# Optimization experiments

Measured on AMD Instinct MI355X. Metric: run time of the kernel, lower is better.

## Reference

```python
import jax, jax.numpy as jnp
import numpy as np
from jax import lax

B, T, N, FI, FO, K = 32, 128, 200, 32, 64, 3
STRIDE, PAD, DIL = 1, 1, 1


def setup_inputs() -> dict:
    key = jax.random.key(0)
    k1, k2, k3 = jax.random.split(key, 3)
    bound = 1.0 / np.sqrt(FI * K)
    x = jax.random.normal(k1, (B, T, N, FI), dtype=jnp.float32)
    weight = jax.random.uniform(k2, (N * FO, FI, K), dtype=jnp.float32,
                                minval=-bound, maxval=bound)
    bias = jax.random.uniform(k3, (N, FO), dtype=jnp.float32,
                              minval=-bound, maxval=bound)
    return {"x": x, "weight": weight, "bias": bias}


def reference(x, weight, bias):
    # x: [B, T, N, FI] -> [B, N*FI, T]   (rearrange '... t n f -> ... (n f) t')
    b, t, n, fi = x.shape
    fo = bias.shape[1]
    xc = jnp.transpose(x, (0, 2, 3, 1)).reshape(b, n * fi, t)
    # Grouped conv1d: one group per instance (n groups), weight [N*FO, FI, K]
    out = lax.conv_general_dilated(
        xc, weight,
        window_strides=(STRIDE,),
        padding=[(PAD, PAD)],
        rhs_dilation=(DIL,),
        feature_group_count=n,
        dimension_numbers=("NCH", "OIH", "NCH"),
    )  # [B, N*FO, T_out]
    t_out = out.shape[-1]
    # rearrange '... (n f) t -> ... t n f'
    out = jnp.transpose(out.reshape(b, n, fo, t_out), (0, 3, 1, 2))
    return out + bias  # bias broadcasts over [B, T_out, N, FO]
```

## Files before the change

### kernel.cpp

```cpp
#include <hip/hip_runtime.h>
#include <hip/hip_bf16.h>
#include <cstddef>

#define B_ 32
#define T_ 128
#define N_ 200
#define FI_ 32
#define FO_ 64
#define K_ 3

typedef __attribute__((ext_vector_type(8))) short short8;
typedef __attribute__((ext_vector_type(8))) unsigned short ushort8;
typedef __attribute__((ext_vector_type(4))) float f32x4;

#define AROW_ 40
#define A_ROWS_ (T_ + 2)
#define B_OFF_ (A_ROWS_ * AROW_)
#define BROW_ 40
#define BK_SZ_ (FO_ * BROW_)

__device__ __forceinline__ unsigned short f2bf(float f) {
    union { __hip_bfloat16 h; unsigned short u; } cv;
    cv.h = __float2bfloat16(f);
    return cv.u;
}

__global__ __launch_bounds__(256, 4) void multiconv_mfma(
    const float* __restrict__ x, const float* __restrict__ w,
    const float* __restrict__ bias, float* __restrict__ out)
{
    __shared__ __align__(16) unsigned short lds[B_OFF_ + K_ * BK_SZ_];

    const int bid = blockIdx.x;
    const int b = bid & 31;
    const int n = bid >> 5;
    const int tid = threadIdx.x;
    const int lane = tid & 63;
    const int wv = tid >> 6;

    const float* xb = x + ((size_t)b * T_ * N_ + n) * FI_;
    for (int s = tid; s < A_ROWS_ * 4; s += 256) {
        const int rr = s >> 2, q = s & 3;
        const int t = rr - 1;
        ushort8 u = (ushort8)0;
        if (t >= 0 && t < T_) {
            const float4 v0 = *reinterpret_cast<const float4*>(
                &xb[(size_t)t * N_ * FI_ + q * 8]);
            const float4 v1 = *reinterpret_cast<const float4*>(
                &xb[(size_t)t * N_ * FI_ + q * 8 + 4]);
            u[0] = f2bf(v0.x); u[1] = f2bf(v0.y); u[2] = f2bf(v0.z); u[3] = f2bf(v0.w);
            u[4] = f2bf(v1.x); u[5] = f2bf(v1.y); u[6] = f2bf(v1.z); u[7] = f2bf(v1.w);
        }
        *reinterpret_cast<ushort8*>(&lds[rr * AROW_ + q * 8]) = u;
    }

    {
        const int f = tid >> 2;
        const int i0 = (tid & 3) * 8;
        const float* wp = w + ((size_t)n * FO_ + f) * (FI_ * K_) + (size_t)i0 * K_;
        float v[24];
        #pragma unroll
        for (int j = 0; j < 6; ++j) {
            const float4 t4 = *reinterpret_cast<const float4*>(&wp[j * 4]);
            v[j*4+0] = t4.x; v[j*4+1] = t4.y; v[j*4+2] = t4.z; v[j*4+3] = t4.w;
        }
        #pragma unroll
        for (int k = 0; k < K_; ++k) {
            ushort8 u;
            #pragma unroll
            for (int j = 0; j < 8; ++j) u[j] = f2bf(v[j * K_ + k]);
            *reinterpret_cast<ushort8*>(&lds[B_OFF_ + k * BK_SZ_ + f * BROW_ + i0]) = u;
        }
    }

    __syncthreads();

    f32x4 acc[2][4];
    #pragma unroll
    for (int m = 0; m < 2; ++m)
        #pragma unroll
        for (int j = 0; j < 4; ++j)
            acc[m][j] = (f32x4){0.f, 0.f, 0.f, 0.f};

    const int row16 = lane & 15;
    const int grp = lane >> 4;

    #pragma unroll
    for (int k = 0; k < K_; ++k) {
        const short8 a0 = *reinterpret_cast<const short8*>(
            &lds[(wv * 32 + 0  + row16 + k) * AROW_ + grp * 8]);
        const short8 a1 = *reinterpret_cast<const short8*>(
            &lds[(wv * 32 + 16 + row16 + k) * AROW_ + grp * 8]);
        #pragma unroll
        for (int j = 0; j < 4; ++j) {
            const short8 bf = *reinterpret_cast<const short8*>(
                &lds[B_OFF_ + k * BK_SZ_ + (j * 16 + row16) * BROW_ + grp * 8]);
            acc[0][j] = __builtin_amdgcn_mfma_f32_16x16x32_bf16(a0, bf, acc[0][j], 0, 0, 0);
            acc[1][j] = __builtin_amdgcn_mfma_f32_16x16x32_bf16(a1, bf, acc[1][j], 0, 0, 0);
        }
    }

    #pragma unroll
    for (int j = 0; j < 4; ++j) {
        const float bv = bias[n * FO_ + j * 16 + row16];
        #pragma unroll
        for (int m = 0; m < 2; ++m) {
            #pragma unroll
            for (int r = 0; r < 4; ++r) {
                const int t = wv * 32 + m * 16 + grp * 4 + r;
                out[(((size_t)b * T_ + t) * N_ + n) * FO_ + j * 16 + row16] =
                    acc[m][j][r] + bv;
            }
        }
    }
}

extern "C" void kernel_launch(void* const* d_in, const int* in_sizes, int n_in,
                              void* d_out, int out_size, void* d_ws, size_t ws_size,
                              hipStream_t stream) {
    const float* x    = (const float*)d_in[0];
    const float* w    = (const float*)d_in[1];
    const float* bias = (const float*)d_in[2];
    float* out = (float*)d_out;

    const int grid = B_ * N_;
    multiconv_mfma<<<grid, 256, 0, stream>>>(x, w, bias, out);
}
```

Baseline: 78.59 us.

## Process two batches per block with double-buffered input prefetch

Each block now handles two batch elements for one instance. The weight tile is converted to bf16 once and reused for both, halving weight loading and conversion. The second batch's input is loaded into registers while the first tile is computed, then written to a second LDS buffer. This halves the grid size and raises LDS use and register pressure (six float4 prefetch registers), which may reduce occupancy.

```diff
diff --git a/kernel.cpp b/kernel.cpp
--- a/kernel.cpp
+++ b/kernel.cpp
@@ -8,6 +8,7 @@
 #define FI_ 32
 #define FO_ 64
 #define K_ 3
+#define NB_ 2
 
 typedef __attribute__((ext_vector_type(8))) short short8;
 typedef __attribute__((ext_vector_type(8))) unsigned short ushort8;
@@ -15,14 +16,62 @@
 
 #define AROW_ 40
 #define A_ROWS_ (T_ + 2)
-#define B_OFF_ (A_ROWS_ * AROW_)
+#define ABUF_ (A_ROWS_ * AROW_)
+#define B_OFF_ (2 * ABUF_)
 #define BROW_ 40
 #define BK_SZ_ (FO_ * BROW_)
+#define NSLOT_ (A_ROWS_ * 4)
 
 __device__ __forceinline__ unsigned short f2bf(float f) {
     union { __hip_bfloat16 h; unsigned short u; } cv;
     cv.h = __float2bfloat16(f);
     return cv.u;
+}
+
+__device__ __forceinline__ f32x4 mfma16(short8 a, short8 b, f32x4 c) {
+    return __builtin_amdgcn_mfma_f32_16x16x32_bf16(a, b, c, 0, 0, 0);
+}
+
+__device__ __forceinline__ void compute_tile(
+    const unsigned short* __restrict__ lds, int abase,
+    int wv, int lane, f32x4 acc[2][4])
+{
+    const int row16 = lane & 15;
+    const int grp = lane >> 4;
+    #pragma unroll
+    for (int k = 0; k < K_; ++k) {
+        const short8 a0 = *reinterpret_cast<const short8*>(
+            &lds[abase + (wv * 32 + 0  + row16 + k) * AROW_ + grp * 8]);
+        const short8 a1 = *reinterpret_cast<const short8*>(
+            &lds[abase + (wv * 32 + 16 + row16 + k) * AROW_ + grp * 8]);
+        #pragma unroll
+        for (int j = 0; j < 4; ++j) {
+            const short8 bf = *reinterpret_cast<const short8*>(
+                &lds[B_OFF_ + k * BK_SZ_ + (j * 16 + row16) * BROW_ + grp * 8]);
+            acc[0][j] = mfma16(a0, bf, acc[0][j]);
+            acc[1][j] = mfma16(a1, bf, acc[1][j]);
+        }
+    }
+}
+
+__device__ __forceinline__ void store_tile(
+    float* __restrict__ out, int b, int n, int wv, int lane,
+    const float bvj[4], f32x4 acc[2][4])
+{
+    const int row16 = lane & 15;
+    const int grp = lane >> 4;
+    #pragma unroll
+    for (int j = 0; j < 4; ++j) {
+        #pragma unroll
+        for (int m = 0; m < 2; ++m) {
+            #pragma unroll
+            for (int r = 0; r < 4; ++r) {
+                const int t = wv * 32 + m * 16 + grp * 4 + r;
+                out[(((size_t)b * T_ + t) * N_ + n) * FO_ + j * 16 + row16] =
+                    acc[m][j][r] + bvj[j];
+            }
+        }
+    }
 }
 
 __global__ __launch_bounds__(256, 4) void multiconv_mfma(
@@ -32,27 +81,13 @@
     __shared__ __align__(16) unsigned short lds[B_OFF_ + K_ * BK_SZ_];
 
     const int bid = blockIdx.x;
-    const int b = bid & 31;
-    const int n = bid >> 5;
+    const int n = bid % N_;
+    const int bp = bid / N_;
+    const int b0 = bp * NB_;
+    const int b1 = b0 + 1;
     const int tid = threadIdx.x;
     const int lane = tid & 63;
     const int wv = tid >> 6;
-
-    const float* xb = x + ((size_t)b * T_ * N_ + n) * FI_;
-    for (int s = tid; s < A_ROWS_ * 4; s += 256) {
-        const int rr = s >> 2, q = s & 3;
-        const int t = rr - 1;
-        ushort8 u = (ushort8)0;
-        if (t >= 0 && t < T_) {
-            const float4 v0 = *reinterpret_cast<const float4*>(
-                &xb[(size_t)t * N_ * FI_ + q * 8]);
-            const float4 v1 = *reinterpret_cast<const float4*>(
-                &xb[(size_t)t * N_ * FI_ + q * 8 + 4]);
-            u[0] = f2bf(v0.x); u[1] = f2bf(v0.y); u[2] = f2bf(v0.z); u[3] = f2bf(v0.w);
-            u[4] = f2bf(v1.x); u[5] = f2bf(v1.y); u[6] = f2bf(v1.z); u[7] = f2bf(v1.w);
-        }
-        *reinterpret_cast<ushort8*>(&lds[rr * AROW_ + q * 8]) = u;
-    }
 
     {
         const int f = tid >> 2;
@@ -73,46 +108,83 @@
         }
     }
 
+    const float* xb0 = x + ((size_t)b0 * T_ * N_ + n) * FI_;
+    const float* xb1 = x + ((size_t)b1 * T_ * N_ + n) * FI_;
+    #pragma unroll
+    for (int ss = 0; ss < 3; ++ss) {
+        const int s = tid + ss * 256;
+        if (ss < 2 || tid < NSLOT_ - 512) {
+            const int rr = s >> 2, q = s & 3;
+            const int t = rr - 1;
+            ushort8 u = (ushort8)0;
+            if (t >= 0 && t < T_) {
+                const float4 v0 = *reinterpret_cast<const float4*>(
+                    &xb0[(size_t)t * N_ * FI_ + q * 8]);
+                const float4 v1 = *reinterpret_cast<const float4*>(
+                    &xb0[(size_t)t * N_ * FI_ + q * 8 + 4]);
+                u[0] = f2bf(v0.x); u[1] = f2bf(v0.y); u[2] = f2bf(v0.z); u[3] = f2bf(v0.w);
+                u[4] = f2bf(v1.x); u[5] = f2bf(v1.y); u[6] = f2bf(v1.z); u[7] = f2bf(v1.w);
+            }
+            *reinterpret_cast<ushort8*>(&lds[rr * AROW_ + q * 8]) = u;
+        }
+    }
+
     __syncthreads();
 
+    float4 nv[6];
+    #pragma unroll
+    for (int ss = 0; ss < 3; ++ss) {
+        const int s = tid + ss * 256;
+        if (ss < 2 || tid < NSLOT_ - 512) {
+            const int rr = s >> 2, q = s & 3;
+            const int t = rr - 1;
+            if (t >= 0 && t < T_) {
+                nv[ss*2]   = *reinterpret_cast<const float4*>(
+                    &xb1[(size_t)t * N_ * FI_ + q * 8]);
+                nv[ss*2+1] = *reinterpret_cast<const float4*>(
+                    &xb1[(size_t)t * N_ * FI_ + q * 8 + 4]);
+            }
+        }
+    }
+
+    const int row16 = lane & 15;
+    float bvj[4];
+    #pragma unroll
+    for (int j = 0; j < 4; ++j) bvj[j] = bias[n * FO_ + j * 16 + row16];
+
     f32x4 acc[2][4];
     #pragma unroll
     for (int m = 0; m < 2; ++m)
         #pragma unroll
-        for (int j = 0; j < 4; ++j)
-            acc[m][j] = (f32x4){0.f, 0.f, 0.f, 0.f};
-
-    const int row16 = lane & 15;
-    const int grp = lane >> 4;
-
-    #pragma unroll
-    for (int k = 0; k < K_; ++k) {
-        const short8 a0 = *reinterpret_cast<const short8*>(
-            &lds[(wv * 32 + 0  + row16 + k) * AROW_ + grp * 8]);
-        const short8 a1 = *reinterpret_cast<const short8*>(
-            &lds[(wv * 32 + 16 + row16 + k) * AROW_ + grp * 8]);
-        #pragma unroll
-        for (int j = 0; j < 4; ++j) {
-            const short8 bf = *reinterpret_cast<const short8*>(
-                &lds[B_OFF_ + k * BK_SZ_ + (j * 16 + row16) * BROW_ + grp * 8]);
-            acc[0][j] = __builtin_amdgcn_mfma_f32_16x16x32_bf16(a0, bf, acc[0][j], 0, 0, 0);
-            acc[1][j] = __builtin_amdgcn_mfma_f32_16x16x32_bf16(a1, bf, acc[1][j], 0, 0, 0);
-        }
-    }
-
-    #pragma unroll
-    for (int j = 0; j < 4; ++j) {
-        const float bv = bias[n * FO_ + j * 16 + row16];
-        #pragma unroll
-        for (int m = 0; m < 2; ++m) {
-            #pragma unroll
-            for (int r = 0; r < 4; ++r) {
-                const int t = wv * 32 + m * 16 + grp * 4 + r;
-                out[(((size_t)b * T_ + t) * N_ + n) * FO_ + j * 16 + row16] =
-                    acc[m][j][r] + bv;
-            }
-        }
-    }
+        for (int j = 0; j < 4; ++j) acc[m][j] = (f32x4){0.f, 0.f, 0.f, 0.f};
+    compute_tile(lds, 0, wv, lane, acc);
+
+    #pragma unroll
+    for (int ss = 0; ss < 3; ++ss) {
+        const int s = tid + ss * 256;
+        if (ss < 2 || tid < NSLOT_ - 512) {
+            const int rr = s >> 2, q = s & 3;
+            const int t = rr - 1;
+            ushort8 u = (ushort8)0;
+            if (t >= 0 && t < T_) {
+                const float4 v0 = nv[ss*2], v1 = nv[ss*2+1];
+                u[0] = f2bf(v0.x); u[1] = f2bf(v0.y); u[2] = f2bf(v0.z); u[3] = f2bf(v0.w);
+                u[4] = f2bf(v1.x); u[5] = f2bf(v1.y); u[6] = f2bf(v1.z); u[7] = f2bf(v1.w);
+            }
+            *reinterpret_cast<ushort8*>(&lds[ABUF_ + rr * AROW_ + q * 8]) = u;
+        }
+    }
+
+    store_tile(out, b0, n, wv, lane, bvj, acc);
+
+    __syncthreads();
+
+    #pragma unroll
+    for (int m = 0; m < 2; ++m)
+        #pragma unroll
+        for (int j = 0; j < 4; ++j) acc[m][j] = (f32x4){0.f, 0.f, 0.f, 0.f};
+    compute_tile(lds, ABUF_, wv, lane, acc);
+    store_tile(out, b1, n, wv, lane, bvj, acc);
 }
 
 extern "C" void kernel_launch(void* const* d_in, const int* in_sizes, int n_in,
@@ -123,6 +195,6 @@
     const float* bias = (const float*)d_in[2];
     float* out = (float*)d_out;
 
-    const int grid = B_ * N_;
+    const int grid = (B_ / NB_) * N_;
     multiconv_mfma<<<grid, 256, 0, stream>>>(x, w, bias, out);
 }
```

New measurement: 89.48 us. 13.8% more time.

## Pre-convert weights to bf16 and tile conv by time chunks without LDS

Applied to the files above, without the earlier changes.

Adds a prep kernel that converts the weights once per call into a bf16 layout in the workspace, arranged per tap. The main kernel is retiled so each block covers a 16-step time chunk for 25 instances, with each wave looping over instances. Each wave loads its A and B fragments straight from global memory into registers, dropping LDS and __syncthreads. The aim is better output-write locality and no per-block weight conversion, at the cost of an extra launch, re-reading x for each tap, and possible wave imbalance (25 instances over 4 waves).

```diff
diff --git a/kernel.cpp b/kernel.cpp
--- a/kernel.cpp
+++ b/kernel.cpp
@@ -8,16 +8,12 @@
 #define FI_ 32
 #define FO_ 64
 #define K_ 3
+#define TT_ 16
+#define NPB_ 25
 
 typedef __attribute__((ext_vector_type(8))) short short8;
 typedef __attribute__((ext_vector_type(8))) unsigned short ushort8;
 typedef __attribute__((ext_vector_type(4))) float f32x4;
-
-#define AROW_ 40
-#define A_ROWS_ (T_ + 2)
-#define B_OFF_ (A_ROWS_ * AROW_)
-#define BROW_ 40
-#define BK_SZ_ (FO_ * BROW_)
 
 __device__ __forceinline__ unsigned short f2bf(float f) {
     union { __hip_bfloat16 h; unsigned short u; } cv;
@@ -25,91 +21,109 @@
     return cv.u;
 }
 
-__global__ __launch_bounds__(256, 4) void multiconv_mfma(
+__global__ void conv_prep(const float* __restrict__ w,
+                          unsigned short* __restrict__ wbf) {
+    const int idx = blockIdx.x * 256 + threadIdx.x;
+    if (idx >= N_ * FO_) return;
+    const float* wp = w + (size_t)idx * (FI_ * K_);
+    float v[FI_ * K_];
+    #pragma unroll
+    for (int j = 0; j < (FI_ * K_) / 4; ++j) {
+        const float4 t4 = *reinterpret_cast<const float4*>(&wp[j * 4]);
+        v[j*4+0] = t4.x; v[j*4+1] = t4.y; v[j*4+2] = t4.z; v[j*4+3] = t4.w;
+    }
+    const int n = idx >> 6, f = idx & 63;
+    #pragma unroll
+    for (int tap = 0; tap < K_; ++tap) {
+        ushort8 u[4];
+        #pragma unroll
+        for (int i = 0; i < FI_; ++i) u[i >> 3][i & 7] = f2bf(v[i * K_ + tap]);
+        unsigned short* dst = wbf + (((size_t)n * K_ + tap) * FO_ + f) * FI_;
+        #pragma unroll
+        for (int q = 0; q < 4; ++q)
+            *reinterpret_cast<ushort8*>(&dst[q * 8]) = u[q];
+    }
+}
+
+template <bool PREW>
+__global__ __launch_bounds__(256, 4) void conv_main(
     const float* __restrict__ x, const float* __restrict__ w,
+    const unsigned short* __restrict__ wbf,
     const float* __restrict__ bias, float* __restrict__ out)
 {
-    __shared__ __align__(16) unsigned short lds[B_OFF_ + K_ * BK_SZ_];
+    const int bid = blockIdx.x;
+    const int nq = bid & 7;
+    const int tt = (bid >> 3) & 7;
+    const int b  = bid >> 6;
+    const int t0 = tt * TT_;
+    const int lane  = threadIdx.x & 63;
+    const int wv    = threadIdx.x >> 6;
+    const int row16 = lane & 15;
+    const int grp   = lane >> 4;
 
-    const int bid = blockIdx.x;
-    const int b = bid & 31;
-    const int n = bid >> 5;
-    const int tid = threadIdx.x;
-    const int lane = tid & 63;
-    const int wv = tid >> 6;
+    #pragma unroll 1
+    for (int i = wv; i < NPB_; i += 4) {
+        const int n = nq * NPB_ + i;
 
-    const float* xb = x + ((size_t)b * T_ * N_ + n) * FI_;
-    for (int s = tid; s < A_ROWS_ * 4; s += 256) {
-        const int rr = s >> 2, q = s & 3;
-        const int t = rr - 1;
-        ushort8 u = (ushort8)0;
-        if (t >= 0 && t < T_) {
-            const float4 v0 = *reinterpret_cast<const float4*>(
-                &xb[(size_t)t * N_ * FI_ + q * 8]);
-            const float4 v1 = *reinterpret_cast<const float4*>(
-                &xb[(size_t)t * N_ * FI_ + q * 8 + 4]);
-            u[0] = f2bf(v0.x); u[1] = f2bf(v0.y); u[2] = f2bf(v0.z); u[3] = f2bf(v0.w);
-            u[4] = f2bf(v1.x); u[5] = f2bf(v1.y); u[6] = f2bf(v1.z); u[7] = f2bf(v1.w);
+        short8 afr[K_];
+        #pragma unroll
+        for (int tap = 0; tap < K_; ++tap) {
+            const int t = t0 + row16 + tap - 1;
+            ushort8 u = (ushort8)0;
+            if (t >= 0 && t < T_) {
+                const float* xp = &x[(((size_t)b * T_ + t) * N_ + n) * FI_ + grp * 8];
+                const float4 v0 = *reinterpret_cast<const float4*>(xp);
+                const float4 v1 = *reinterpret_cast<const float4*>(xp + 4);
+                u[0] = f2bf(v0.x); u[1] = f2bf(v0.y); u[2] = f2bf(v0.z); u[3] = f2bf(v0.w);
+                u[4] = f2bf(v1.x); u[5] = f2bf(v1.y); u[6] = f2bf(v1.z); u[7] = f2bf(v1.w);
+            }
+            union { ushort8 u8; short8 s8; } cv; cv.u8 = u;
+            afr[tap] = cv.s8;
         }
-        *reinterpret_cast<ushort8*>(&lds[rr * AROW_ + q * 8]) = u;
-    }
 
-    {
-        const int f = tid >> 2;
-        const int i0 = (tid & 3) * 8;
-        const float* wp = w + ((size_t)n * FO_ + f) * (FI_ * K_) + (size_t)i0 * K_;
-        float v[24];
+        f32x4 acc[4];
         #pragma unroll
-        for (int j = 0; j < 6; ++j) {
-            const float4 t4 = *reinterpret_cast<const float4*>(&wp[j * 4]);
-            v[j*4+0] = t4.x; v[j*4+1] = t4.y; v[j*4+2] = t4.z; v[j*4+3] = t4.w;
-        }
-        #pragma unroll
-        for (int k = 0; k < K_; ++k) {
-            ushort8 u;
-            #pragma unroll
-            for (int j = 0; j < 8; ++j) u[j] = f2bf(v[j * K_ + k]);
-            *reinterpret_cast<ushort8*>(&lds[B_OFF_ + k * BK_SZ_ + f * BROW_ + i0]) = u;
-        }
-    }
+        for (int j = 0; j < 4; ++j) acc[j] = (f32x4){0.f, 0.f, 0.f, 0.f};
 
-    __syncthreads();
-
-    f32x4 acc[2][4];
-    #pragma unroll
-    for (int m = 0; m < 2; ++m)
-        #pragma unroll
-        for (int j = 0; j < 4; ++j)
-            acc[m][j] = (f32x4){0.f, 0.f, 0.f, 0.f};
-
-    const int row16 = lane & 15;
-    const int grp = lane >> 4;
-
-    #pragma unroll
-    for (int k = 0; k < K_; ++k) {
-        const short8 a0 = *reinterpret_cast<const short8*>(
-            &lds[(wv * 32 + 0  + row16 + k) * AROW_ + grp * 8]);
-        const short8 a1 = *reinterpret_cast<const short8*>(
-            &lds[(wv * 32 + 16 + row16 + k) * AROW_ + grp * 8]);
         #pragma unroll
         for (int j = 0; j < 4; ++j) {
-            const short8 bf = *reinterpret_cast<const short8*>(
-                &lds[B_OFF_ + k * BK_SZ_ + (j * 16 + row16) * BROW_ + grp * 8]);
-            acc[0][j] = __builtin_amdgcn_mfma_f32_16x16x32_bf16(a0, bf, acc[0][j], 0, 0, 0);
-            acc[1][j] = __builtin_amdgcn_mfma_f32_16x16x32_bf16(a1, bf, acc[1][j], 0, 0, 0);
+            short8 bfr[K_];
+            if constexpr (PREW) {
+                #pragma unroll
+                for (int tap = 0; tap < K_; ++tap)
+                    bfr[tap] = *reinterpret_cast<const short8*>(
+                        &wbf[(((size_t)n * K_ + tap) * FO_ + j * 16 + row16) * FI_ + grp * 8]);
+            } else {
+                const float* wp = &w[((size_t)(n * FO_ + j * 16 + row16)) * (FI_ * K_) + grp * 24];
+                float v[24];
+                #pragma unroll
+                for (int q = 0; q < 6; ++q) {
+                    const float4 t4 = *reinterpret_cast<const float4*>(&wp[q * 4]);
+                    v[q*4+0] = t4.x; v[q*4+1] = t4.y; v[q*4+2] = t4.z; v[q*4+3] = t4.w;
+                }
+                #pragma unroll
+                for (int tap = 0; tap < K_; ++tap) {
+                    ushort8 u;
+                    #pragma unroll
+                    for (int e = 0; e < 8; ++e) u[e] = f2bf(v[e * K_ + tap]);
+                    union { ushort8 u8; short8 s8; } cv; cv.u8 = u;
+                    bfr[tap] = cv.s8;
+                }
+            }
+            #pragma unroll
+            for (int tap = 0; tap < K_; ++tap)
+                acc[j] = __builtin_amdgcn_mfma_f32_16x16x32_bf16(
+                    afr[tap], bfr[tap], acc[j], 0, 0, 0);
         }
-    }
 
-    #pragma unroll
-    for (int j = 0; j < 4; ++j) {
-        const float bv = bias[n * FO_ + j * 16 + row16];
         #pragma unroll
-        for (int m = 0; m < 2; ++m) {
+        for (int j = 0; j < 4; ++j) {
+            const float bv = bias[n * FO_ + j * 16 + row16];
             #pragma unroll
             for (int r = 0; r < 4; ++r) {
-                const int t = wv * 32 + m * 16 + grp * 4 + r;
+                const int t = t0 + grp * 4 + r;
                 out[(((size_t)b * T_ + t) * N_ + n) * FO_ + j * 16 + row16] =
-                    acc[m][j][r] + bv;
+                    acc[j][r] + bv;
             }
         }
     }
@@ -123,6 +137,14 @@
     const float* bias = (const float*)d_in[2];
     float* out = (float*)d_out;
 
-    const int grid = B_ * N_;
-    multiconv_mfma<<<grid, 256, 0, stream>>>(x, w, bias, out);
+    const size_t W_BF_BYTES = (size_t)N_ * K_ * FO_ * FI_ * 2;
+    const int grid = B_ * (T_ / TT_) * 8;
+
+    if (ws_size >= W_BF_BYTES) {
+        unsigned short* wbf = (unsigned short*)d_ws;
+        conv_prep<<<(N_ * FO_ + 255) / 256, 256, 0, stream>>>(w, wbf);
+        conv_main<true><<<grid, 256, 0, stream>>>(x, w, wbf, bias, out);
+    } else {
+        conv_main<false><<<grid, 256, 0, stream>>>(x, w, nullptr, bias, out);
+    }
 }
```

Result: slower. 152.3 us (+93.7%).
